# Optimization experiments

Hardware: AMD Instinct MI355X
Metric: run time of the kernel (lower is better)

The kernel has to match this reference:

```python
import jax, jax.numpy as jnp
import numpy as np

B, N, M = 2, 4096, 4096
DQ = DKV = DOUT = 512
HEADS, DH = 8, 64
INNER = HEADS * DH
SCALE = DH ** -0.5


def _ln(x, g, b, eps=1e-5):
    mu = jnp.mean(x, axis=-1, keepdims=True)
    var = jnp.mean(jnp.square(x - mu), axis=-1, keepdims=True)
    return (x - mu) * jax.lax.rsqrt(var + eps) * g + b


def setup_inputs() -> dict:
    key = jax.random.key(0)
    ks = jax.random.split(key, 12)
    s = lambda fan: 1.0 / np.sqrt(fan)
    return {
        "q0": jax.random.normal(ks[0], (B, N, DQ), jnp.float32),
        "kv0": jax.random.normal(ks[1], (B, M, DKV), jnp.float32),
        "normq_g": jnp.ones((DQ,), jnp.float32),
        "normq_b": jnp.zeros((DQ,), jnp.float32),
        "normkv_g": jnp.ones((DKV,), jnp.float32),
        "normkv_b": jnp.zeros((DKV,), jnp.float32),
        "Wq": jax.random.normal(ks[2], (DQ, INNER), jnp.float32) * s(DQ),
        "Wk": jax.random.normal(ks[3], (DKV, INNER), jnp.float32) * s(DKV),
        "Wv": jax.random.normal(ks[4], (DKV, INNER), jnp.float32) * s(DKV),
        "Wr": jax.random.normal(ks[5], (INNER, DQ), jnp.float32) * s(INNER),
        "mlp_g": jnp.ones((DQ,), jnp.float32),
        "mlp_b": jnp.zeros((DQ,), jnp.float32),
        "W1": jax.random.normal(ks[6], (DQ, DOUT), jnp.float32) * s(DQ),
        "b1": jnp.zeros((DOUT,), jnp.float32),
        "W2": jax.random.normal(ks[7], (DOUT, DOUT), jnp.float32) * s(DOUT),
        "b2": jnp.zeros((DOUT,), jnp.float32),
    }


def reference(q0, kv0, normq_g, normq_b, normkv_g, normkv_b,
              Wq, Wk, Wv, Wr, mlp_g, mlp_b, W1, b1, W2, b2):
    # projections
    q = _ln(q0, normq_g, normq_b) @ Wq                    # [B,N,INNER]
    kv = _ln(kv0, normkv_g, normkv_b)                     # [B,M,DKV]
    k = kv @ Wk                                           # [B,M,INNER]
    v = kv @ Wv                                           # [B,M,INNER]
    # split heads: b n (h d) -> b h n d
    q = q.reshape(B, N, HEADS, DH).transpose(0, 2, 1, 3)
    k = k.reshape(B, M, HEADS, DH).transpose(0, 2, 1, 3)
    v = v.reshape(B, M, HEADS, DH).transpose(0, 2, 1, 3)
    dots = jnp.einsum('bhnd,bhmd->bhnm', q, k) * SCALE    # [B,H,N,M]
    attn = jax.nn.softmax(dots, axis=-1)
    out = jnp.einsum('bhnm,bhmd->bhnd', attn, v)          # [B,H,N,DH]
    out = out.transpose(0, 2, 1, 3).reshape(B, N, INNER)  # b h n d -> b n (h d)
    out = out @ Wr + q0                                   # [B,N,DQ]
    # MLP branch with residual
    h = _ln(out, mlp_g, mlp_b)
    h = jax.nn.relu(h @ W1 + b1) @ W2 + b2
    return out + h
```

## Files before the change

### kernel.cpp

```cpp
#include <hip/hip_runtime.h>

typedef unsigned short u16;
typedef unsigned int u32;
typedef __bf16 bf16x8 __attribute__((ext_vector_type(8)));
typedef float f32x4 __attribute__((ext_vector_type(4)));
typedef u16 u16x8 __attribute__((ext_vector_type(8)));

#define SC2 0.18033688011112042f

__device__ __forceinline__ u16 bf16rne(float f) {
  u32 u = __float_as_uint(f);
  u32 r = (u + 0x7FFFu + ((u >> 16) & 1u)) >> 16;
  return (u16)r;
}
__device__ __forceinline__ u32 packrne(float a, float b) {
  return (u32)bf16rne(a) | ((u32)bf16rne(b) << 16);
}

__device__ __forceinline__ void async16(const void* g, void* l) {
  __builtin_amdgcn_global_load_lds(
      (__attribute__((address_space(1))) void*)(g),
      (__attribute__((address_space(3))) void*)(l), 16, 0, 0);
}
__device__ __forceinline__ void wait_vm0() {
  asm volatile("s_waitcnt vmcnt(0)" ::: "memory");
}

__global__ __launch_bounds__(256) void wtrans_kernel(
    const float* __restrict__ w0, const float* __restrict__ w1,
    const float* __restrict__ w2, const float* __restrict__ w3,
    const float* __restrict__ w4, const float* __restrict__ w5,
    u16* __restrict__ out) {
  __shared__ u16 T[64 * 72];
  int t = threadIdx.x;
  int widx = blockIdx.y;
  int k0 = (blockIdx.x & 7) * 64, n0 = (blockIdx.x >> 3) * 64;
  const float* W = w0;
  if (widx == 1) W = w1; else if (widx == 2) W = w2; else if (widx == 3) W = w3;
  else if (widx == 4) W = w4; else if (widx == 5) W = w5;
#pragma unroll
  for (int p = 0; p < 4; ++p) {
    int kr = p * 16 + (t >> 4);
    int nc = (t & 15) * 4;
    float4 v = *(const float4*)(W + (size_t)(k0 + kr) * 512 + n0 + nc);
    T[(nc + 0) * 72 + kr] = bf16rne(v.x);
    T[(nc + 1) * 72 + kr] = bf16rne(v.y);
    T[(nc + 2) * 72 + kr] = bf16rne(v.z);
    T[(nc + 3) * 72 + kr] = bf16rne(v.w);
  }
  __syncthreads();
  u16* ob = out + (size_t)widx * 262144;
#pragma unroll
  for (int p = 0; p < 2; ++p) {
    int idx = p * 256 + t;
    int nr = idx >> 3, ch = idx & 7;
    uint4 val = *(const uint4*)(T + nr * 72 + ch * 8);
    *(uint4*)(ob + (size_t)(n0 + nr) * 512 + k0 + ch * 8) = val;
  }
}

__device__ __forceinline__ void ln_row(const float* xr, const float* gp,
                                       const float* bp, u16* orow, int lane) {
  const float* xl = xr + lane * 8;
  float4 a0 = *(const float4*)xl;
  float4 a1 = *(const float4*)(xl + 4);
  float v[8] = {a0.x, a0.y, a0.z, a0.w, a1.x, a1.y, a1.z, a1.w};
  float s = 0.f, s2 = 0.f;
#pragma unroll
  for (int j = 0; j < 8; ++j) { s += v[j]; s2 += v[j] * v[j]; }
#pragma unroll
  for (int off = 32; off; off >>= 1) {
    s += __shfl_xor(s, off);
    s2 += __shfl_xor(s2, off);
  }
  float mu = s * (1.0f / 512.0f);
  float rstd = rsqrtf(s2 * (1.0f / 512.0f) - mu * mu + 1e-5f);
  const float* gl = gp + lane * 8;
  const float* bl = bp + lane * 8;
  float4 g0 = *(const float4*)gl, g1 = *(const float4*)(gl + 4);
  float4 b0 = *(const float4*)bl, b1 = *(const float4*)(bl + 4);
  float gg[8] = {g0.x, g0.y, g0.z, g0.w, g1.x, g1.y, g1.z, g1.w};
  float bb[8] = {b0.x, b0.y, b0.z, b0.w, b1.x, b1.y, b1.z, b1.w};
  u16x8 ov;
#pragma unroll
  for (int j = 0; j < 8; ++j) ov[j] = bf16rne((v[j] - mu) * rstd * gg[j] + bb[j]);
  *(u16x8*)(orow + lane * 8) = ov;
}

__global__ __launch_bounds__(256) void ln_kernel(
    const float* __restrict__ x, const float* __restrict__ g,
    const float* __restrict__ b, u16* __restrict__ o) {
  int w = threadIdx.x >> 6, lane = threadIdx.x & 63;
  size_t row = (size_t)blockIdx.x * 4 + w;
  ln_row(x + row * 512, g, b, o + row * 512, lane);
}

__global__ __launch_bounds__(256) void ln2_kernel(
    const float* __restrict__ x0, const float* __restrict__ g0,
    const float* __restrict__ b0, u16* __restrict__ o0,
    const float* __restrict__ x1, const float* __restrict__ g1,
    const float* __restrict__ b1, u16* __restrict__ o1) {
  int w = threadIdx.x >> 6, lane = threadIdx.x & 63;
  size_t row = (size_t)blockIdx.x * 4 + w;
  if (row < 8192) {
    ln_row(x0 + row * 512, g0, b0, o0 + row * 512, lane);
  } else {
    size_t r2 = row - 8192;
    ln_row(x1 + r2 * 512, g1, b1, o1 + r2 * 512, lane);
  }
}

template <int MODE>
__global__ __launch_bounds__(256) void gemm512_kernel(
    const u16* __restrict__ A, const u16* __restrict__ Bt, void* __restrict__ Cv,
    void* __restrict__ Cv2, const float* __restrict__ bias,
    const float* __restrict__ res) {
  __shared__ __align__(16) u16 As[2][4096];
  __shared__ __align__(16) u16 Bs[2][2048];
  const int t = threadIdx.x;
  const int lane = t & 63;
  const int w = t >> 6;
  const int row0 = blockIdx.y * 128;
  const int col0 = blockIdx.x * 64;
  f32x4 acc[2][4];
#pragma unroll
  for (int i = 0; i < 2; ++i)
#pragma unroll
    for (int j = 0; j < 4; ++j) acc[i][j] = (f32x4){0.f, 0.f, 0.f, 0.f};

#define GSTAGE(buf, k0)                                                          \
  {                                                                              \
    _Pragma("unroll") for (int i = 0; i < 2; ++i) {                              \
      int s = t + 256 * i;                                                       \
      int mts = s >> 6, L = s & 63;                                              \
      async16(A + (size_t)(row0 + mts * 16 + (L & 15)) * 512 + (k0) + (L >> 4) * 8, \
              (char*)As[buf] + s * 16);                                          \
    }                                                                            \
    {                                                                            \
      int s = t;                                                                 \
      int nts = s >> 6, L = s & 63;                                              \
      async16(Bt + (size_t)(col0 + nts * 16 + (L & 15)) * 512 + (k0) + (L >> 4) * 8, \
              (char*)Bs[buf] + s * 16);                                          \
    }                                                                            \
  }

  GSTAGE(0, 0);
  wait_vm0();
  __syncthreads();

  for (int kk = 0; kk < 16; ++kk) {
    if (kk < 15) GSTAGE((kk + 1) & 1, (kk + 1) * 32);
    const u16* Ac = As[kk & 1];
    const u16* Bc = Bs[kk & 1];
    bf16x8 Af[2], Bf[4];
#pragma unroll
    for (int mt = 0; mt < 2; ++mt)
      Af[mt] = *(const bf16x8*)(Ac + ((w * 2 + mt) * 64 + lane) * 8);
#pragma unroll
    for (int nt = 0; nt < 4; ++nt)
      Bf[nt] = *(const bf16x8*)(Bc + (nt * 64 + lane) * 8);
#pragma unroll
    for (int mt = 0; mt < 2; ++mt)
#pragma unroll
      for (int nt = 0; nt < 4; ++nt)
        acc[mt][nt] = __builtin_amdgcn_mfma_f32_16x16x32_bf16(Af[mt], Bf[nt], acc[mt][nt], 0, 0, 0);
    wait_vm0();
    __syncthreads();
  }

  const int q = lane >> 4, cl = lane & 15;
#pragma unroll
  for (int mt = 0; mt < 2; ++mt) {
#pragma unroll
    for (int nt = 0; nt < 4; ++nt) {
      int col = col0 + nt * 16 + cl;
#pragma unroll
      for (int r = 0; r < 4; ++r) {
        int row = row0 + (w * 2 + mt) * 16 + q * 4 + r;
        float v = acc[mt][nt][r];
        if (MODE == 0) {
          ((u16*)Cv)[(size_t)row * 512 + col] = bf16rne(v);
        } else if (MODE == 1) {
          size_t idx = (size_t)row * 512 + col;
          ((float*)Cv)[idx] = v + res[idx];
        } else if (MODE == 2) {
          v += bias[col];
          ((u16*)Cv)[(size_t)row * 512 + col] = bf16rne(fmaxf(v, 0.f));
        } else if (MODE == 3) {
          size_t idx = (size_t)row * 512 + col;
          ((float*)Cv)[idx] = v + bias[col] + res[idx];
        } else if (MODE == 4) {
          ((u16*)Cv)[(size_t)row * 512 + col] = bf16rne(v * SC2);
        } else {
          u16* D = (col < 512) ? (u16*)Cv : (u16*)Cv2;
          ((u16*)D)[(size_t)row * 512 + (col & 511)] = bf16rne(v);
        }
      }
    }
  }
}

__global__ __launch_bounds__(256) void vtrans_kernel(const u16* __restrict__ V,
                                                     u16* __restrict__ VT) {
  __shared__ u16 Ts[64 * 65];
  int t = threadIdx.x;
  int mi = blockIdx.x, di = blockIdx.y, b = blockIdx.z;
  const u16* Vb = V + (size_t)b * 4096 * 512;
  u16* VTb = VT + (size_t)b * 512 * 4096;
#pragma unroll
  for (int p = 0; p < 2; ++p) {
    int r = p * 32 + (t >> 3);
    int c = (t & 7) * 8;
    u16x8 vv = *(const u16x8*)(Vb + (size_t)(mi * 64 + r) * 512 + di * 64 + c);
#pragma unroll
    for (int j = 0; j < 8; ++j) Ts[r * 65 + c + j] = vv[j];
  }
  __syncthreads();
#pragma unroll
  for (int p = 0; p < 2; ++p) {
    int rr = p * 32 + (t >> 3);
    int cc = (t & 7) * 8;
    u16x8 ov;
#pragma unroll
    for (int j = 0; j < 8; ++j) ov[j] = Ts[(cc + j) * 65 + rr];
    *(u16x8*)(VTb + (size_t)(di * 64 + rr) * 4096 + mi * 64 + cc) = ov;
  }
}

__global__ __launch_bounds__(256, 4) void attn_kernel(
    const u16* __restrict__ Q, const u16* __restrict__ K,
    const u16* __restrict__ VT, u16* __restrict__ O) {
  __shared__ __align__(16) u16 QP[4096];
  __shared__ __align__(16) u16 Ks[2][4096];
  __shared__ __align__(16) u16 Vs[2][4096];
  const int t = threadIdx.x;
  const int lane = t & 63;
  const int w = t >> 6;
  const int g = lane >> 4, cl = lane & 15;
  const int qt = blockIdx.x, h = blockIdx.y, b = blockIdx.z;
  const u16* Qg = Q + ((size_t)(b * 4096 + qt * 64)) * 512 + h * 64;
  const u16* Kg = K + ((size_t)b * 4096) * 512 + h * 64;
  const u16* VTg = VT + ((size_t)(b * 512 + h * 64)) * 4096;
  u16* Og = O + ((size_t)(b * 4096 + qt * 64)) * 512 + h * 64;
  char* Pw = (char*)QP + w * 2048;

#pragma unroll
  for (int i = 0; i < 2; ++i) {
    int s = t + 256 * i;
    int c = s >> 6, L = s & 63;
    async16(Qg + (size_t)((c >> 1) * 16 + (L & 15)) * 512 + (c & 1) * 32 + (L >> 4) * 8,
            (char*)QP + s * 16);
  }
#pragma unroll
  for (int i = 0; i < 2; ++i) {
    int s = t + 256 * i;
    int c = s >> 6, L = s & 63;
    async16(Kg + (size_t)((c >> 1) * 16 + (L & 15)) * 512 + (c & 1) * 32 + (L >> 4) * 8,
            (char*)Ks[0] + s * 16);
    async16(VTg + (size_t)((c >> 1) * 16 + (L & 15)) * 4096 + (c & 1) * 32 + (L >> 4) * 8,
            (char*)Vs[0] + s * 16);
  }
  wait_vm0();
  __syncthreads();

  bf16x8 Qb[2];
#pragma unroll
  for (int ks = 0; ks < 2; ++ks)
    Qb[ks] = *(const bf16x8*)((char*)QP + (w * 2 + ks) * 1024 + lane * 16);

  u16x8 ou;
#pragma unroll
  for (int j = 0; j < 8; ++j) ou[j] = 0x3F80;
  bf16x8 ones = __builtin_bit_cast(bf16x8, ou);

  f32x4 Oa[4], lsum = (f32x4){0.f, 0.f, 0.f, 0.f};
#pragma unroll
  for (int i = 0; i < 4; ++i) Oa[i] = (f32x4){0.f, 0.f, 0.f, 0.f};

  const int sw = (cl >> 1) & 3;

  for (int it = 0; it < 64; ++it) {
    if (it < 63) {
      int m0n = (it + 1) * 64;
      int nb = (it + 1) & 1;
#pragma unroll
      for (int i = 0; i < 2; ++i) {
        int s = t + 256 * i;
        int c = s >> 6, L = s & 63;
        async16(Kg + (size_t)(m0n + (c >> 1) * 16 + (L & 15)) * 512 + (c & 1) * 32 + (L >> 4) * 8,
                (char*)Ks[nb] + s * 16);
        async16(VTg + (size_t)((c >> 1) * 16 + (L & 15)) * 4096 + m0n + (c & 1) * 32 + (L >> 4) * 8,
                (char*)Vs[nb] + s * 16);
      }
    }
    const u16* Kc = Ks[it & 1];
    const u16* Vc = Vs[it & 1];

    f32x4 St[4];
#pragma unroll
    for (int mt = 0; mt < 4; ++mt) St[mt] = (f32x4){0.f, 0.f, 0.f, 0.f};
#pragma unroll
    for (int ks = 0; ks < 2; ++ks)
#pragma unroll
      for (int mt = 0; mt < 4; ++mt) {
        bf16x8 Ka = *(const bf16x8*)((const char*)Kc + ((mt * 2 + ks) * 64 + lane) * 16);
        St[mt] = __builtin_amdgcn_mfma_f32_16x16x32_bf16(Ka, Qb[ks], St[mt], 0, 0, 0);
      }

#pragma unroll
    for (int mt = 0; mt < 4; ++mt) {
      float p0 = __builtin_amdgcn_exp2f(St[mt][0]);
      float p1 = __builtin_amdgcn_exp2f(St[mt][1]);
      float p2 = __builtin_amdgcn_exp2f(St[mt][2]);
      float p3 = __builtin_amdgcn_exp2f(St[mt][3]);
      uint2 pk;
      pk.x = __builtin_amdgcn_perm(__float_as_uint(p1), __float_as_uint(p0), 0x07060302u);
      pk.y = __builtin_amdgcn_perm(__float_as_uint(p3), __float_as_uint(p2), 0x07060302u);
      *(uint2*)(Pw + (((g >> 1) * 256 + cl * 16 + ((mt ^ sw) << 2) + ((g & 1) << 1)) << 2)) = pk;
    }

    bf16x8 Pb[2];
#pragma unroll
    for (int ks = 0; ks < 2; ++ks)
      Pb[ks] = *(const bf16x8*)(Pw + (((g & 1) * 256 + cl * 16 +
                                       (((ks * 2 + (g >> 1)) ^ sw) << 2)) << 2));

#pragma unroll
    for (int ks = 0; ks < 2; ++ks) {
      lsum = __builtin_amdgcn_mfma_f32_16x16x32_bf16(ones, Pb[ks], lsum, 0, 0, 0);
#pragma unroll
      for (int mt = 0; mt < 4; ++mt) {
        bf16x8 Va = *(const bf16x8*)((const char*)Vc + ((mt * 2 + ks) * 64 + lane) * 16);
        Oa[mt] = __builtin_amdgcn_mfma_f32_16x16x32_bf16(Va, Pb[ks], Oa[mt], 0, 0, 0);
      }
    }
    wait_vm0();
    __syncthreads();
  }

  float inv = 1.0f / lsum[0];
#pragma unroll
  for (int mt = 0; mt < 4; ++mt) {
    uint2 pk;
    pk.x = packrne(Oa[mt][0] * inv, Oa[mt][1] * inv);
    pk.y = packrne(Oa[mt][2] * inv, Oa[mt][3] * inv);
    *(uint2*)(Pw + ((cl * 32 + ((mt ^ (cl & 3)) << 3) + (g << 1)) << 2)) = pk;
  }
#pragma unroll
  for (int p = 0; p < 2; ++p) {
    int idx = p * 64 + lane;
    int q = idx >> 3, c = idx & 7;
    uint4 val = *(const uint4*)(Pw + ((q * 32 + (((c >> 1) ^ (q & 3)) << 3) + ((c & 1) << 2)) << 2));
    *(uint4*)(Og + (size_t)(w * 16 + q) * 512 + c * 8) = val;
  }
}

extern "C" void kernel_launch(void* const* d_in, const int* in_sizes, int n_in,
                              void* d_out, int out_size, void* d_ws, size_t ws_size,
                              hipStream_t stream) {
  const float* q0 = (const float*)d_in[0];
  const float* kv0 = (const float*)d_in[1];
  const float* nq_g = (const float*)d_in[2];
  const float* nq_b = (const float*)d_in[3];
  const float* nkv_g = (const float*)d_in[4];
  const float* nkv_b = (const float*)d_in[5];
  const float* Wq = (const float*)d_in[6];
  const float* Wk = (const float*)d_in[7];
  const float* Wv = (const float*)d_in[8];
  const float* Wr = (const float*)d_in[9];
  const float* mlp_g = (const float*)d_in[10];
  const float* mlp_b = (const float*)d_in[11];
  const float* W1 = (const float*)d_in[12];
  const float* b1 = (const float*)d_in[13];
  const float* W2 = (const float*)d_in[14];
  const float* b2 = (const float*)d_in[15];
  float* out = (float*)d_out;

  char* ws = (char*)d_ws;
  u16* qn = (u16*)(ws + 0);
  u16* kvn = (u16*)(ws + 8388608);
  u16* Qp = (u16*)(ws + 16777216);
  u16* Kp = (u16*)(ws + 25165824);
  u16* Vp = (u16*)(ws + 33554432);
  u16* VT = (u16*)(ws + 41943040);
  float* ob = (float*)(ws + 50331648);
  u16* wb = (u16*)(ws + 67108864);
  u16* wqT = wb;
  u16* wkT = wb + 262144;
  u16* wrT = wb + 786432;
  u16* w1T = wb + 1048576;
  u16* w2T = wb + 1310720;

  dim3 blk(256);
  wtrans_kernel<<<dim3(64, 6), blk, 0, stream>>>(Wq, Wk, Wv, Wr, W1, W2, wb);
  ln2_kernel<<<4096, blk, 0, stream>>>(q0, nq_g, nq_b, qn, kv0, nkv_g, nkv_b, kvn);
  gemm512_kernel<4><<<dim3(8, 64), blk, 0, stream>>>(qn, wqT, Qp, nullptr, nullptr, nullptr);
  gemm512_kernel<5><<<dim3(16, 64), blk, 0, stream>>>(kvn, wkT, Kp, Vp, nullptr, nullptr);
  vtrans_kernel<<<dim3(64, 8, 2), blk, 0, stream>>>(Vp, VT);
  attn_kernel<<<dim3(64, 8, 2), blk, 0, stream>>>(Qp, Kp, VT, Vp );
  gemm512_kernel<1><<<dim3(8, 64), blk, 0, stream>>>(Vp, wrT, ob, nullptr, nullptr, q0);
  ln_kernel<<<2048, blk, 0, stream>>>(ob, mlp_g, mlp_b, kvn );
  gemm512_kernel<2><<<dim3(8, 64), blk, 0, stream>>>(kvn, w1T, qn , nullptr, b1, nullptr);
  gemm512_kernel<3><<<dim3(8, 64), blk, 0, stream>>>(qn, w2T, out, nullptr, b2, ob);
}
```

Baseline: 349.9 us.

## Split-KV attention with larger per-wave query tiles, fused V transpose, finer waits

The attention kernel now gives each wave 64 queries instead of 16, so every K/V fragment loaded from LDS feeds four times as many MFMAs. The key dimension is split in two across blocks, and a new combine kernel sums the two partial outputs and divides by the summed row sums. The K/V projection GEMM writes V directly in transposed layout, which removes the separate transpose kernel. The GEMM and attention loops switch from a full vmcnt(0) wait to partial waits with a raw s_barrier so the next stage's loads can stay in flight. The split adds an extra kernel and bf16 partial-output round trips, the larger tiles raise register pressure, and the workspace buffers are reshuffled with aliasing.

```diff
diff --git a/kernel.cpp b/kernel.cpp
--- a/kernel.cpp
+++ b/kernel.cpp
@@ -16,14 +16,24 @@
 __device__ __forceinline__ u32 packrne(float a, float b) {
   return (u32)bf16rne(a) | ((u32)bf16rne(b) << 16);
 }
+__device__ __forceinline__ float b2f(u16 v) {
+  return __uint_as_float(((u32)v) << 16);
+}
 
 __device__ __forceinline__ void async16(const void* g, void* l) {
   __builtin_amdgcn_global_load_lds(
       (__attribute__((address_space(1))) void*)(g),
       (__attribute__((address_space(3))) void*)(l), 16, 0, 0);
 }
-__device__ __forceinline__ void wait_vm0() {
-  asm volatile("s_waitcnt vmcnt(0)" ::: "memory");
+template <int N>
+__device__ __forceinline__ void vm_wait() {
+  asm volatile("s_waitcnt vmcnt(%0)" ::"n"(N) : "memory");
+}
+__device__ __forceinline__ void lgkm_wait0() {
+  asm volatile("s_waitcnt lgkmcnt(0)" ::: "memory");
+}
+__device__ __forceinline__ void bar() {
+  asm volatile("s_barrier" ::: "memory");
 }
 
 __global__ __launch_bounds__(256) void wtrans_kernel(
@@ -145,11 +155,15 @@
   }
 
   GSTAGE(0, 0);
-  wait_vm0();
-  __syncthreads();
 
   for (int kk = 0; kk < 16; ++kk) {
-    if (kk < 15) GSTAGE((kk + 1) & 1, (kk + 1) * 32);
+    if (kk < 15) {
+      GSTAGE((kk + 1) & 1, (kk + 1) * 32);
+      vm_wait<3>();
+    } else {
+      vm_wait<0>();
+    }
+    bar();
     const u16* Ac = As[kk & 1];
     const u16* Bc = Bs[kk & 1];
     bf16x8 Af[2], Bf[4];
@@ -164,8 +178,7 @@
 #pragma unroll
       for (int nt = 0; nt < 4; ++nt)
         acc[mt][nt] = __builtin_amdgcn_mfma_f32_16x16x32_bf16(Af[mt], Bf[nt], acc[mt][nt], 0, 0, 0);
-    wait_vm0();
-    __syncthreads();
+    bar();
   }
 
   const int q = lane >> 4, cl = lane & 15;
@@ -174,11 +187,21 @@
 #pragma unroll
     for (int nt = 0; nt < 4; ++nt) {
       int col = col0 + nt * 16 + cl;
+      if (MODE == 6 && col >= 512) {
+        int d = col - 512;
+        int bb = row0 >> 12;
+        int mloc = (row0 & 4095) + (w * 2 + mt) * 16 + q * 4;
+        uint2 pk;
+        pk.x = packrne(acc[mt][nt][0], acc[mt][nt][1]);
+        pk.y = packrne(acc[mt][nt][2], acc[mt][nt][3]);
+        *(uint2*)((u16*)Cv2 + ((size_t)bb * 512 + d) * 4096 + mloc) = pk;
+        continue;
+      }
 #pragma unroll
       for (int r = 0; r < 4; ++r) {
         int row = row0 + (w * 2 + mt) * 16 + q * 4 + r;
         float v = acc[mt][nt][r];
-        if (MODE == 0) {
+        if (MODE == 0 || MODE == 6) {
           ((u16*)Cv)[(size_t)row * 512 + col] = bf16rne(v);
         } else if (MODE == 1) {
           size_t idx = (size_t)row * 512 + col;
@@ -191,168 +214,165 @@
           ((float*)Cv)[idx] = v + bias[col] + res[idx];
         } else if (MODE == 4) {
           ((u16*)Cv)[(size_t)row * 512 + col] = bf16rne(v * SC2);
-        } else {
-          u16* D = (col < 512) ? (u16*)Cv : (u16*)Cv2;
-          ((u16*)D)[(size_t)row * 512 + (col & 511)] = bf16rne(v);
         }
       }
     }
   }
 }
 
-__global__ __launch_bounds__(256) void vtrans_kernel(const u16* __restrict__ V,
-                                                     u16* __restrict__ VT) {
-  __shared__ u16 Ts[64 * 65];
-  int t = threadIdx.x;
-  int mi = blockIdx.x, di = blockIdx.y, b = blockIdx.z;
-  const u16* Vb = V + (size_t)b * 4096 * 512;
-  u16* VTb = VT + (size_t)b * 512 * 4096;
-#pragma unroll
-  for (int p = 0; p < 2; ++p) {
-    int r = p * 32 + (t >> 3);
-    int c = (t & 7) * 8;
-    u16x8 vv = *(const u16x8*)(Vb + (size_t)(mi * 64 + r) * 512 + di * 64 + c);
-#pragma unroll
-    for (int j = 0; j < 8; ++j) Ts[r * 65 + c + j] = vv[j];
-  }
-  __syncthreads();
-#pragma unroll
-  for (int p = 0; p < 2; ++p) {
-    int rr = p * 32 + (t >> 3);
-    int cc = (t & 7) * 8;
-    u16x8 ov;
-#pragma unroll
-    for (int j = 0; j < 8; ++j) ov[j] = Ts[(cc + j) * 65 + rr];
-    *(u16x8*)(VTb + (size_t)(di * 64 + rr) * 4096 + mi * 64 + cc) = ov;
-  }
-}
-
-__global__ __launch_bounds__(256, 4) void attn_kernel(
+__global__ __launch_bounds__(128, 2) void attn_kernel(
     const u16* __restrict__ Q, const u16* __restrict__ K,
-    const u16* __restrict__ VT, u16* __restrict__ O) {
-  __shared__ __align__(16) u16 QP[4096];
+    const u16* __restrict__ VT, u16* __restrict__ O0, u16* __restrict__ O1,
+    float* __restrict__ lpart) {
   __shared__ __align__(16) u16 Ks[2][4096];
   __shared__ __align__(16) u16 Vs[2][4096];
+  __shared__ __align__(16) u16 Ps[2][1024];
   const int t = threadIdx.x;
   const int lane = t & 63;
   const int w = t >> 6;
   const int g = lane >> 4, cl = lane & 15;
-  const int qt = blockIdx.x, h = blockIdx.y, b = blockIdx.z;
-  const u16* Qg = Q + ((size_t)(b * 4096 + qt * 64)) * 512 + h * 64;
-  const u16* Kg = K + ((size_t)b * 4096) * 512 + h * 64;
-  const u16* VTg = VT + ((size_t)(b * 512 + h * 64)) * 4096;
-  u16* Og = O + ((size_t)(b * 4096 + qt * 64)) * 512 + h * 64;
-  char* Pw = (char*)QP + w * 2048;
-
-#pragma unroll
-  for (int i = 0; i < 2; ++i) {
-    int s = t + 256 * i;
-    int c = s >> 6, L = s & 63;
-    async16(Qg + (size_t)((c >> 1) * 16 + (L & 15)) * 512 + (c & 1) * 32 + (L >> 4) * 8,
-            (char*)QP + s * 16);
-  }
-#pragma unroll
-  for (int i = 0; i < 2; ++i) {
-    int s = t + 256 * i;
-    int c = s >> 6, L = s & 63;
-    async16(Kg + (size_t)((c >> 1) * 16 + (L & 15)) * 512 + (c & 1) * 32 + (L >> 4) * 8,
-            (char*)Ks[0] + s * 16);
-    async16(VTg + (size_t)((c >> 1) * 16 + (L & 15)) * 4096 + (c & 1) * 32 + (L >> 4) * 8,
-            (char*)Vs[0] + s * 16);
-  }
-  wait_vm0();
-  __syncthreads();
-
-  bf16x8 Qb[2];
-#pragma unroll
-  for (int ks = 0; ks < 2; ++ks)
-    Qb[ks] = *(const bf16x8*)((char*)QP + (w * 2 + ks) * 1024 + lane * 16);
+  const int qt = blockIdx.x, h = blockIdx.y;
+  const int b = blockIdx.z >> 1, sp = blockIdx.z & 1;
+  const u16* Qg = Q + ((size_t)(b * 4096 + qt * 128 + w * 64)) * 512 + h * 64;
+  const u16* Kg = K + ((size_t)(b * 4096 + sp * 2048)) * 512 + h * 64;
+  const u16* VTg = VT + ((size_t)(b * 512 + h * 64)) * 4096 + sp * 2048;
+  u16* Ob = (sp ? O1 : O0) + (((size_t)(b * 8 + h) * 4096) + qt * 128 + w * 64) * 64;
+  float* lb = lpart + ((size_t)((sp * 2 + b) * 8 + h)) * 4096 + qt * 128 + w * 64;
+  char* Pw = (char*)Ps[w];
+
+#pragma unroll
+  for (int i = 0; i < 8; ++i) {
+    async16(Qg + (size_t)((i >> 1) * 16 + cl) * 512 + (i & 1) * 32 + g * 8,
+            (char*)Ks[w] + (i * 64 + lane) * 16);
+  }
+  vm_wait<0>();
+  bf16x8 Qb[4][2];
+#pragma unroll
+  for (int nt = 0; nt < 4; ++nt)
+#pragma unroll
+    for (int ks = 0; ks < 2; ++ks)
+      Qb[nt][ks] = *(const bf16x8*)((char*)Ks[w] + ((nt * 2 + ks) * 64 + lane) * 16);
+  lgkm_wait0();
+  bar();
+
+#define STAGEKV(buf, m0)                                                          \
+  {                                                                               \
+    _Pragma("unroll") for (int i = 0; i < 4; ++i) {                               \
+      int s = t + 128 * i; int c = s >> 6; int L = s & 63;                        \
+      async16(Kg + (size_t)((m0) + (c >> 1) * 16 + (L & 15)) * 512 + (c & 1) * 32 + (L >> 4) * 8, \
+              (char*)Ks[buf] + s * 16);                                           \
+    }                                                                             \
+    _Pragma("unroll") for (int i = 0; i < 4; ++i) {                               \
+      int s = t + 128 * i; int c = s >> 6; int L = s & 63;                        \
+      async16(VTg + (size_t)((c >> 1) * 16 + (L & 15)) * 4096 + (m0) + (c & 1) * 32 + (L >> 4) * 8, \
+              (char*)Vs[buf] + s * 16);                                           \
+    }                                                                             \
+  }
+
+  STAGEKV(0, 0);
 
   u16x8 ou;
 #pragma unroll
   for (int j = 0; j < 8; ++j) ou[j] = 0x3F80;
   bf16x8 ones = __builtin_bit_cast(bf16x8, ou);
 
-  f32x4 Oa[4], lsum = (f32x4){0.f, 0.f, 0.f, 0.f};
-#pragma unroll
-  for (int i = 0; i < 4; ++i) Oa[i] = (f32x4){0.f, 0.f, 0.f, 0.f};
-
-  const int sw = (cl >> 1) & 3;
-
-  for (int it = 0; it < 64; ++it) {
-    if (it < 63) {
-      int m0n = (it + 1) * 64;
-      int nb = (it + 1) & 1;
-#pragma unroll
-      for (int i = 0; i < 2; ++i) {
-        int s = t + 256 * i;
-        int c = s >> 6, L = s & 63;
-        async16(Kg + (size_t)(m0n + (c >> 1) * 16 + (L & 15)) * 512 + (c & 1) * 32 + (L >> 4) * 8,
-                (char*)Ks[nb] + s * 16);
-        async16(VTg + (size_t)((c >> 1) * 16 + (L & 15)) * 4096 + m0n + (c & 1) * 32 + (L >> 4) * 8,
-                (char*)Vs[nb] + s * 16);
-      }
+  f32x4 Oa[4][4], ls[4];
+#pragma unroll
+  for (int i = 0; i < 4; ++i) {
+    ls[i] = (f32x4){0.f, 0.f, 0.f, 0.f};
+#pragma unroll
+    for (int j = 0; j < 4; ++j) Oa[i][j] = (f32x4){0.f, 0.f, 0.f, 0.f};
+  }
+  const int s7 = cl & 7;
+
+  for (int it = 0; it < 32; ++it) {
+    if (it < 31) {
+      STAGEKV((it + 1) & 1, (it + 1) * 64);
+      vm_wait<8>();
+    } else {
+      vm_wait<0>();
     }
+    bar();
     const u16* Kc = Ks[it & 1];
     const u16* Vc = Vs[it & 1];
-
-    f32x4 St[4];
-#pragma unroll
-    for (int mt = 0; mt < 4; ++mt) St[mt] = (f32x4){0.f, 0.f, 0.f, 0.f};
-#pragma unroll
-    for (int ks = 0; ks < 2; ++ks)
+    bf16x8 Kf[4][2], Vf[4][2];
+#pragma unroll
+    for (int mt = 0; mt < 4; ++mt)
+#pragma unroll
+      for (int ks = 0; ks < 2; ++ks) {
+        Kf[mt][ks] = *(const bf16x8*)((const char*)Kc + ((mt * 2 + ks) * 64 + lane) * 16);
+        Vf[mt][ks] = *(const bf16x8*)((const char*)Vc + ((mt * 2 + ks) * 64 + lane) * 16);
+      }
+
+#pragma unroll
+    for (int nt = 0; nt < 4; ++nt) {
+      f32x4 St[4];
+#pragma unroll
+      for (int mt = 0; mt < 4; ++mt) St[mt] = (f32x4){0.f, 0.f, 0.f, 0.f};
+#pragma unroll
+      for (int ks = 0; ks < 2; ++ks)
+#pragma unroll
+        for (int mt = 0; mt < 4; ++mt)
+          St[mt] = __builtin_amdgcn_mfma_f32_16x16x32_bf16(Kf[mt][ks], Qb[nt][ks], St[mt], 0, 0, 0);
+
 #pragma unroll
       for (int mt = 0; mt < 4; ++mt) {
-        bf16x8 Ka = *(const bf16x8*)((const char*)Kc + ((mt * 2 + ks) * 64 + lane) * 16);
-        St[mt] = __builtin_amdgcn_mfma_f32_16x16x32_bf16(Ka, Qb[ks], St[mt], 0, 0, 0);
+        float p0 = __builtin_amdgcn_exp2f(St[mt][0]);
+        float p1 = __builtin_amdgcn_exp2f(St[mt][1]);
+        float p2 = __builtin_amdgcn_exp2f(St[mt][2]);
+        float p3 = __builtin_amdgcn_exp2f(St[mt][3]);
+        uint2 pk;
+        pk.x = __builtin_amdgcn_perm(__float_as_uint(p1), __float_as_uint(p0), 0x07060302u);
+        pk.y = __builtin_amdgcn_perm(__float_as_uint(p3), __float_as_uint(p2), 0x07060302u);
+        *(uint2*)(Pw + cl * 128 + (((mt * 2 + (g >> 1)) ^ s7) << 4) + ((g & 1) << 3)) = pk;
       }
-
-#pragma unroll
-    for (int mt = 0; mt < 4; ++mt) {
-      float p0 = __builtin_amdgcn_exp2f(St[mt][0]);
-      float p1 = __builtin_amdgcn_exp2f(St[mt][1]);
-      float p2 = __builtin_amdgcn_exp2f(St[mt][2]);
-      float p3 = __builtin_amdgcn_exp2f(St[mt][3]);
+      bf16x8 Pb[2];
+#pragma unroll
+      for (int ks = 0; ks < 2; ++ks)
+        Pb[ks] = *(const bf16x8*)(Pw + cl * 128 + (((ks * 4 + g) ^ s7) << 4));
+      ls[nt] = __builtin_amdgcn_mfma_f32_16x16x32_bf16(ones, Pb[0], ls[nt], 0, 0, 0);
+      ls[nt] = __builtin_amdgcn_mfma_f32_16x16x32_bf16(ones, Pb[1], ls[nt], 0, 0, 0);
+#pragma unroll
+      for (int ks = 0; ks < 2; ++ks)
+#pragma unroll
+        for (int mtd = 0; mtd < 4; ++mtd)
+          Oa[mtd][nt] = __builtin_amdgcn_mfma_f32_16x16x32_bf16(Vf[mtd][ks], Pb[ks], Oa[mtd][nt], 0, 0, 0);
+    }
+    bar();
+  }
+
+#pragma unroll
+  for (int nt = 0; nt < 4; ++nt) {
+    int q = nt * 16 + cl;
+#pragma unroll
+    for (int mtd = 0; mtd < 4; ++mtd) {
       uint2 pk;
-      pk.x = __builtin_amdgcn_perm(__float_as_uint(p1), __float_as_uint(p0), 0x07060302u);
-      pk.y = __builtin_amdgcn_perm(__float_as_uint(p3), __float_as_uint(p2), 0x07060302u);
-      *(uint2*)(Pw + (((g >> 1) * 256 + cl * 16 + ((mt ^ sw) << 2) + ((g & 1) << 1)) << 2)) = pk;
+      pk.x = packrne(Oa[mtd][nt][0], Oa[mtd][nt][1]);
+      pk.y = packrne(Oa[mtd][nt][2], Oa[mtd][nt][3]);
+      *(uint2*)(Ob + (size_t)q * 64 + mtd * 16 + g * 4) = pk;
     }
-
-    bf16x8 Pb[2];
-#pragma unroll
-    for (int ks = 0; ks < 2; ++ks)
-      Pb[ks] = *(const bf16x8*)(Pw + (((g & 1) * 256 + cl * 16 +
-                                       (((ks * 2 + (g >> 1)) ^ sw) << 2)) << 2));
-
-#pragma unroll
-    for (int ks = 0; ks < 2; ++ks) {
-      lsum = __builtin_amdgcn_mfma_f32_16x16x32_bf16(ones, Pb[ks], lsum, 0, 0, 0);
-#pragma unroll
-      for (int mt = 0; mt < 4; ++mt) {
-        bf16x8 Va = *(const bf16x8*)((const char*)Vc + ((mt * 2 + ks) * 64 + lane) * 16);
-        Oa[mt] = __builtin_amdgcn_mfma_f32_16x16x32_bf16(Va, Pb[ks], Oa[mt], 0, 0, 0);
-      }
-    }
-    wait_vm0();
-    __syncthreads();
-  }
-
-  float inv = 1.0f / lsum[0];
-#pragma unroll
-  for (int mt = 0; mt < 4; ++mt) {
-    uint2 pk;
-    pk.x = packrne(Oa[mt][0] * inv, Oa[mt][1] * inv);
-    pk.y = packrne(Oa[mt][2] * inv, Oa[mt][3] * inv);
-    *(uint2*)(Pw + ((cl * 32 + ((mt ^ (cl & 3)) << 3) + (g << 1)) << 2)) = pk;
-  }
-#pragma unroll
-  for (int p = 0; p < 2; ++p) {
-    int idx = p * 64 + lane;
-    int q = idx >> 3, c = idx & 7;
-    uint4 val = *(const uint4*)(Pw + ((q * 32 + (((c >> 1) ^ (q & 3)) << 3) + ((c & 1) << 2)) << 2));
-    *(uint4*)(Og + (size_t)(w * 16 + q) * 512 + c * 8) = val;
-  }
+    if (g == 0) lb[q] = ls[nt][0];
+  }
+}
+
+__global__ __launch_bounds__(256) void combine_kernel(
+    const u16* __restrict__ O0, const u16* __restrict__ O1,
+    const float* __restrict__ lp, u16* __restrict__ out) {
+  int idx = blockIdx.x * 256 + threadIdx.x;
+  int dc = idx & 7;
+  int q = (idx >> 3) & 4095;
+  int h = (idx >> 15) & 7;
+  int b = idx >> 18;
+  size_t po = (((size_t)(b * 8 + h) * 4096) + q) * 64 + dc * 8;
+  u16x8 a = *(const u16x8*)(O0 + po);
+  u16x8 c = *(const u16x8*)(O1 + po);
+  float l0 = lp[((size_t)(b * 8 + h)) * 4096 + q];
+  float l1 = lp[((size_t)(16 + b * 8 + h)) * 4096 + q];
+  float inv = 1.0f / (l0 + l1);
+  u16x8 o;
+#pragma unroll
+  for (int j = 0; j < 8; ++j) o[j] = bf16rne((b2f(a[j]) + b2f(c[j])) * inv);
+  *(u16x8*)(out + ((size_t)(b * 4096 + q)) * 512 + h * 64 + dc * 8) = o;
 }
 
 extern "C" void kernel_launch(void* const* d_in, const int* in_sizes, int n_in,
@@ -377,14 +397,19 @@
   float* out = (float*)d_out;
 
   char* ws = (char*)d_ws;
-  u16* qn = (u16*)(ws + 0);
-  u16* kvn = (u16*)(ws + 8388608);
+  float* ob = (float*)(ws + 0);
+  u16* O1p = (u16*)(ws + 0);
   u16* Qp = (u16*)(ws + 16777216);
+  u16* aout = (u16*)(ws + 16777216);
   u16* Kp = (u16*)(ws + 25165824);
-  u16* Vp = (u16*)(ws + 33554432);
-  u16* VT = (u16*)(ws + 41943040);
-  float* ob = (float*)(ws + 50331648);
-  u16* wb = (u16*)(ws + 67108864);
+  u16* h1 = (u16*)(ws + 25165824);
+  u16* VTp = (u16*)(ws + 33554432);
+  u16* kvn2 = (u16*)(ws + 33554432);
+  u16* wb = (u16*)(ws + 41943040);
+  float* lpart = (float*)(ws + 45088768);
+  u16* qn = (u16*)(ws + 46137344);
+  u16* O0p = (u16*)(ws + 46137344);
+  u16* kvn = (u16*)(ws + 54525952);
   u16* wqT = wb;
   u16* wkT = wb + 262144;
   u16* wrT = wb + 786432;
@@ -395,11 +420,11 @@
   wtrans_kernel<<<dim3(64, 6), blk, 0, stream>>>(Wq, Wk, Wv, Wr, W1, W2, wb);
   ln2_kernel<<<4096, blk, 0, stream>>>(q0, nq_g, nq_b, qn, kv0, nkv_g, nkv_b, kvn);
   gemm512_kernel<4><<<dim3(8, 64), blk, 0, stream>>>(qn, wqT, Qp, nullptr, nullptr, nullptr);
-  gemm512_kernel<5><<<dim3(16, 64), blk, 0, stream>>>(kvn, wkT, Kp, Vp, nullptr, nullptr);
-  vtrans_kernel<<<dim3(64, 8, 2), blk, 0, stream>>>(Vp, VT);
-  attn_kernel<<<dim3(64, 8, 2), blk, 0, stream>>>(Qp, Kp, VT, Vp );
-  gemm512_kernel<1><<<dim3(8, 64), blk, 0, stream>>>(Vp, wrT, ob, nullptr, nullptr, q0);
-  ln_kernel<<<2048, blk, 0, stream>>>(ob, mlp_g, mlp_b, kvn );
-  gemm512_kernel<2><<<dim3(8, 64), blk, 0, stream>>>(kvn, w1T, qn , nullptr, b1, nullptr);
-  gemm512_kernel<3><<<dim3(8, 64), blk, 0, stream>>>(qn, w2T, out, nullptr, b2, ob);
-}
+  gemm512_kernel<6><<<dim3(16, 64), blk, 0, stream>>>(kvn, wkT, Kp, VTp, nullptr, nullptr);
+  attn_kernel<<<dim3(32, 8, 4), dim3(128), 0, stream>>>(Qp, Kp, VTp, O0p, O1p, lpart);
+  combine_kernel<<<2048, blk, 0, stream>>>(O0p, O1p, lpart, aout);
+  gemm512_kernel<1><<<dim3(8, 64), blk, 0, stream>>>(aout, wrT, ob, nullptr, nullptr, q0);
+  ln_kernel<<<2048, blk, 0, stream>>>(ob, mlp_g, mlp_b, kvn2);
+  gemm512_kernel<2><<<dim3(8, 64), blk, 0, stream>>>(kvn2, w1T, h1, nullptr, b1, nullptr);
+  gemm512_kernel<3><<<dim3(8, 64), blk, 0, stream>>>(h1, w2T, out, nullptr, b2, ob);
+}
```

Measured after the change: 294.7 us. 15.8% less time.
